# Kernel optimization log

Measured on AMD Instinct MI355X. Metric: run time of the kernel, lower is better.

## Reference

```python
import jax, jax.numpy as jnp
import numpy as np

_K_MASK = float(jnp.finfo(jnp.float32).min)
EPS = 1e-6
B, T, D = 2, 2048, 2048
NH, NKV, HD = 16, 4, 128


def _rope_tables(key):
    # Standard RoPE tables: (B, T, HD) with [freqs, freqs] layout (rotate_half convention)
    inv_freq = 1.0 / (10000.0 ** (np.arange(0, HD, 2, dtype=np.float32) / HD))  # (HD/2,)
    pos = np.arange(T, dtype=np.float32)
    freqs = np.einsum('t,f->tf', pos, inv_freq)              # (T, HD/2)
    emb = np.concatenate([freqs, freqs], axis=-1)            # (T, HD)
    cos = jnp.broadcast_to(jnp.cos(emb)[None], (B, T, HD))
    sin = jnp.broadcast_to(jnp.sin(emb)[None], (B, T, HD))
    return cos, sin


def setup_inputs() -> dict:
    key = jax.random.key(0)
    ks = jax.random.split(key, 6)
    s = 0.02
    cos, sin = _rope_tables(key)
    return {
        'x': jax.random.normal(ks[0], (B, T, D), jnp.float32),
        'cos': cos,
        'sin': sin,
        'wq': jax.random.normal(ks[1], (D, NH * HD * 2), jnp.float32) * s,
        'wk': jax.random.normal(ks[2], (D, NKV * HD), jnp.float32) * s,
        'wv': jax.random.normal(ks[3], (D, NKV * HD), jnp.float32) * s,
        'wo': jax.random.normal(ks[4], (NH * HD, D), jnp.float32) * s,
        'q_norm_w': jnp.ones((HD,), jnp.float32),
        'k_norm_w': jnp.ones((HD,), jnp.float32),
        'segment_ids': jnp.ones((B, T), jnp.int32),
        'position_ids': jnp.broadcast_to(jnp.arange(T, dtype=jnp.int32)[None], (B, T)),
    }


def _rmsnorm(x, w):
    var = jnp.mean(jnp.square(x.astype(jnp.float32)), axis=-1, keepdims=True)
    return (x.astype(jnp.float32) * jax.lax.rsqrt(var + EPS)).astype(x.dtype) * w


def _rotate_half(x):
    x1, x2 = jnp.split(x, 2, axis=-1)
    return jnp.concatenate([-x2, x1], axis=-1)


def _apply_rope(q, k, cos, sin):
    # q: (B, NH, T, HD), k: (B, NKV, T, HD), cos/sin: (B, T, HD)
    c = cos[:, None, :, :]
    s = sin[:, None, :, :]
    q = q * c + _rotate_half(q) * s
    k = k * c + _rotate_half(k) * s
    return q, k


def reference(x, cos, sin, wq, wk, wv, wo, q_norm_w, k_norm_w, segment_ids, position_ids):
    Bx, Tx, _ = x.shape
    n_rep = NH // NKV
    scale = HD ** -0.5

    q_out = (x @ wq).reshape(Bx, Tx, NH, HD * 2)
    query, gate = jnp.split(q_out, 2, axis=-1)         # each (B, T, NH, HD)
    gate = gate.reshape(Bx, Tx, -1)                    # (B, T, NH*HD)
    query = _rmsnorm(query, q_norm_w).transpose(0, 2, 1, 3)   # (B, NH, T, HD)
    key = _rmsnorm((x @ wk).reshape(Bx, Tx, NKV, HD), k_norm_w).transpose(0, 2, 1, 3)
    value = (x @ wv).reshape(Bx, Tx, NKV, HD).transpose(0, 2, 1, 3)

    query, key = _apply_rope(query, key, cos, sin)
    if n_rep > 1:
        key = jnp.repeat(key, n_rep, axis=1)
        value = jnp.repeat(value, n_rep, axis=1)

    attn_logits = jnp.einsum('bhqd,bhkd->bhqk', query, key) * scale
    causal = position_ids[:, :, None] >= position_ids[:, None, :]
    seg = segment_ids[:, :, None] == segment_ids[:, None, :]
    mask = (causal & seg)[:, None, :, :]
    attn_logits = jnp.where(mask, attn_logits, _K_MASK)
    attn_weights = jax.nn.softmax(attn_logits.astype(jnp.float32), axis=-1).astype(attn_logits.dtype)
    attn_out = jnp.einsum('bhqk,bhkd->bhqd', attn_weights, value)
    attn_out = attn_out.transpose(0, 2, 1, 3).reshape(Bx, Tx, -1)  # (B, T, NH*HD)
    attn_out = attn_out * jax.nn.sigmoid(gate)
    return attn_out @ wo
```

## Files before the change

### kernel.cpp

```cpp
#include <hip/hip_runtime.h>

#define AS1 __attribute__((address_space(1)))
#define AS3 __attribute__((address_space(3)))

typedef __bf16 bf16x8 __attribute__((ext_vector_type(8)));
typedef float f32x4 __attribute__((ext_vector_type(4)));
typedef float f32x16 __attribute__((ext_vector_type(16)));
typedef unsigned short us8 __attribute__((ext_vector_type(8)));
typedef unsigned int u32x4 __attribute__((ext_vector_type(4)));

static constexpr int T_ = 2048;
static constexpr int NH_ = 16;
static constexpr int NKV_ = 4;
static constexpr int HD_ = 128;
static constexpr int NQKV_ = 5120;
static constexpr float SL2E_ = 0.12751744f;

static __device__ __forceinline__ unsigned short f2b(float f) {
  unsigned u = __builtin_bit_cast(unsigned, f);
  u += 0x7fffu + ((u >> 16) & 1u);
  return (unsigned short)(u >> 16);
}
static __device__ __forceinline__ void load_lds16(const void* g, void* l) {
  __builtin_amdgcn_global_load_lds((const AS1 unsigned int*)g, (AS3 unsigned int*)l, 16, 0, 0);
}
static __device__ __forceinline__ f32x4 mfma16(bf16x8 a, bf16x8 b, f32x4 c) {
  return __builtin_amdgcn_mfma_f32_16x16x32_bf16(a, b, c, 0, 0, 0);
}
static __device__ __forceinline__ f32x16 mfma32(bf16x8 a, bf16x8 b, f32x16 c) {
  return __builtin_amdgcn_mfma_f32_32x32x16_bf16(a, b, c, 0, 0, 0);
}
static __device__ __forceinline__ unsigned cvtpk(float lo, float hi) {
  unsigned r;
  asm("v_cvt_pk_bf16_f32 %0, %1, %2" : "=v"(r) : "v"(lo), "v"(hi));
  return r;
}
static __device__ __forceinline__ void pl32swap(unsigned& a, unsigned& b) {
  asm("v_permlane32_swap_b32 %0, %1" : "+v"(a), "+v"(b));
}

__global__ __launch_bounds__(256) void conv_bf16_kernel(
    const float* __restrict__ src, unsigned short* __restrict__ dst, int n) {
  int i = (blockIdx.x * 256 + threadIdx.x) * 4;
  if (i >= n) return;
  float4 v = *(const float4*)(src + i);
  ushort4 o;
  o.x = f2b(v.x); o.y = f2b(v.y); o.z = f2b(v.z); o.w = f2b(v.w);
  *(ushort4*)(dst + i) = o;
}

__global__ void tconv_kernel(const float* __restrict__ src, unsigned short* __restrict__ dst,
                             int R, int C, int roff) {
  __shared__ float tile[32][33];
  const int c0 = blockIdx.x * 32, r0 = blockIdx.y * 32;
#pragma unroll
  for (int j = 0; j < 32; j += 8)
    tile[threadIdx.y + j][threadIdx.x] =
        src[(size_t)(r0 + threadIdx.y + j) * C + c0 + threadIdx.x];
  __syncthreads();
#pragma unroll
  for (int j = 0; j < 32; j += 8)
    dst[(size_t)(roff + c0 + threadIdx.y + j) * R + r0 + threadIdx.x] =
        f2b(tile[threadIdx.x][threadIdx.y + j]);
}

__global__ void vtrans_kernel(const float* __restrict__ qkv, unsigned short* __restrict__ Vt) {
  __shared__ unsigned short tile[32][33];
  const int bh = blockIdx.z;
  const int b = bh >> 2, vh = bh & 3;
  const int d0 = blockIdx.x * 32, t0 = blockIdx.y * 32;
#pragma unroll
  for (int j = 0; j < 32; j += 8) {
    const int t = t0 + threadIdx.y + j;
    tile[threadIdx.y + j][threadIdx.x] =
        f2b(qkv[(size_t)(b * T_ + t) * NQKV_ + 4608 + vh * 128 + d0 + threadIdx.x]);
  }
  __syncthreads();
  unsigned short* dst = Vt + (size_t)bh * HD_ * T_;
#pragma unroll
  for (int j = 0; j < 32; j += 8)
    dst[(size_t)(d0 + threadIdx.y + j) * T_ + t0 + threadIdx.x] =
        tile[threadIdx.x][threadIdx.y + j];
}

__global__ __launch_bounds__(256) void gemm_bt_kernel(
    const unsigned short* __restrict__ A, const unsigned short* __restrict__ Bt,
    float* __restrict__ C, int K, int N) {
  __shared__ __align__(16) unsigned short As[128 * 32];
  __shared__ __align__(16) unsigned short Bs[128 * 32];
  const int tid = threadIdx.x;
  const int wid = tid >> 6, lane = tid & 63;
  const int lq = lane & 15, lg = lane >> 4;
  const int wr = wid >> 1, wc = wid & 1;
  const int brow = blockIdx.y * 128, bcol = blockIdx.x * 128;

  f32x4 acc[4][4];
#pragma unroll
  for (int m = 0; m < 4; ++m)
#pragma unroll
    for (int n = 0; n < 4; ++n) acc[m][n] = (f32x4){0.f, 0.f, 0.f, 0.f};

  for (int k0 = 0; k0 < K; k0 += 32) {
#pragma unroll
    for (int i = 0; i < 2; ++i) {
      const int e = (i * 4 + wid) * 512 + lane * 8;
      const int row = e >> 5, col = e & 31;
      load_lds16(A + (size_t)(brow + row) * K + k0 + col, As + (i * 4 + wid) * 512);
      load_lds16(Bt + (size_t)(bcol + row) * K + k0 + col, Bs + (i * 4 + wid) * 512);
    }
    __syncthreads();
    bf16x8 a[4], bb[4];
#pragma unroll
    for (int m = 0; m < 4; ++m)
      a[m] = *(const bf16x8*)&As[(wr * 64 + m * 16 + lq) * 32 + lg * 8];
#pragma unroll
    for (int n = 0; n < 4; ++n)
      bb[n] = *(const bf16x8*)&Bs[(wc * 64 + n * 16 + lq) * 32 + lg * 8];
#pragma unroll
    for (int m = 0; m < 4; ++m)
#pragma unroll
      for (int n = 0; n < 4; ++n) acc[m][n] = mfma16(a[m], bb[n], acc[m][n]);
    __syncthreads();
  }
#pragma unroll
  for (int m = 0; m < 4; ++m)
#pragma unroll
    for (int n = 0; n < 4; ++n)
#pragma unroll
      for (int r = 0; r < 4; ++r)
        C[(size_t)(brow + wr * 64 + m * 16 + lg * 4 + r) * N + bcol + wc * 64 + n * 16 + lq] =
            acc[m][n][r];
}

__global__ __launch_bounds__(256) void postproc_kernel(
    const float* __restrict__ qkv, const float* __restrict__ cosT,
    const float* __restrict__ sinT, const float* __restrict__ qnw,
    const float* __restrict__ knw, unsigned short* __restrict__ Qg,
    unsigned short* __restrict__ Kg) {
  const int row = blockIdx.x;
  const int b = row >> 11, t = row & 2047;
  const float* src = qkv + (size_t)row * NQKV_;
  const int tid = threadIdx.x;
  const int sub = tid & 15;
  const int i0 = sub * 8;
  const bool lo = sub < 8;

  float cs[8], sn[8];
#pragma unroll
  for (int j = 0; j < 8; ++j) {
    cs[j] = cosT[(size_t)row * HD_ + i0 + j];
    sn[j] = sinT[(size_t)row * HD_ + i0 + j];
  }
  {
    const int h = tid >> 4;
    float q[8], ss = 0.f;
#pragma unroll
    for (int j = 0; j < 8; ++j) { q[j] = src[h * 256 + i0 + j]; ss += q[j] * q[j]; }
    ss += __shfl_xor(ss, 1); ss += __shfl_xor(ss, 2);
    ss += __shfl_xor(ss, 4); ss += __shfl_xor(ss, 8);
    const float rms = rsqrtf(ss * (1.f / 128.f) + 1e-6f);
    float qn[8];
#pragma unroll
    for (int j = 0; j < 8; ++j) qn[j] = q[j] * rms * qnw[i0 + j];
    float pr[8];
#pragma unroll
    for (int j = 0; j < 8; ++j) pr[j] = __shfl_xor(qn[j], 8);
    us8 ov;
#pragma unroll
    for (int j = 0; j < 8; ++j) ov[j] = f2b(qn[j] * cs[j] + (lo ? -pr[j] : pr[j]) * sn[j]);
    *(us8*)(Qg + ((size_t)(b * NH_ + h) * T_ + t) * HD_ + i0) = ov;
  }
  if (tid < 64) {
    const int kh = tid >> 4;
    float k[8], ss = 0.f;
#pragma unroll
    for (int j = 0; j < 8; ++j) { k[j] = src[4096 + kh * 128 + i0 + j]; ss += k[j] * k[j]; }
    ss += __shfl_xor(ss, 1); ss += __shfl_xor(ss, 2);
    ss += __shfl_xor(ss, 4); ss += __shfl_xor(ss, 8);
    const float rms = rsqrtf(ss * (1.f / 128.f) + 1e-6f);
    float kn[8];
#pragma unroll
    for (int j = 0; j < 8; ++j) kn[j] = k[j] * rms * knw[i0 + j];
    float pr[8];
#pragma unroll
    for (int j = 0; j < 8; ++j) pr[j] = __shfl_xor(kn[j], 8);
    us8 ov;
#pragma unroll
    for (int j = 0; j < 8; ++j) ov[j] = f2b(kn[j] * cs[j] + (lo ? -pr[j] : pr[j]) * sn[j]);
    *(us8*)(Kg + ((size_t)(b * NKV_ + kh) * T_ + t) * HD_ + i0) = ov;
  }
}

__global__ __launch_bounds__(256, 2) void attn_kernel(
    const unsigned short* __restrict__ Qg, const unsigned short* __restrict__ Kg,
    const unsigned short* __restrict__ Vt, const float* __restrict__ qkv,
    unsigned short* __restrict__ attnb) {
  __shared__ __align__(16) char smem[65536];
  const int i = blockIdx.x;
  const int xi = (i >> 3) & 15;
  const int grp = (i & 7) + ((i >> 7) << 3);
  const int h = grp & 15, b = grp >> 4;
  const int qt = b ? (15 - xi) : xi;
  const int kh = h >> 2;
  const int tid = threadIdx.x, wid = tid >> 6, lane = tid & 63;
  const int lq = lane & 31, hi = lane >> 5;
  const int q0 = qt * 128;
  const int qbase = q0 + wid * 32;
  const int qrow = qbase + lq;

  bf16x8 qf[8];
  const unsigned short* qptr = Qg + ((size_t)(b * NH_ + h) * T_ + qrow) * HD_;
#pragma unroll
  for (int t = 0; t < 8; ++t) qf[t] = *(const bf16x8*)(qptr + t * 16 + hi * 8);

  const char* Kbase = (const char*)(Kg + (size_t)(b * NKV_ + kh) * T_ * HD_);
  const char* Vbase = (const char*)(Vt + (size_t)(b * NKV_ + kh) * HD_ * T_);

  f32x16 o[4];
#pragma unroll
  for (int d = 0; d < 4; ++d)
#pragma unroll
    for (int r = 0; r < 16; ++r) o[d][r] = 0.f;
  float m_r = -1e30f, l_r = 0.f;
  const int nt = 2 * qt + 2;

  auto STAGE = [&](int tt, int c) {
    const int t0 = tt * 64;
    char* kd = smem + c * 32768;
    char* vd = kd + 16384;
#pragma unroll
    for (int j = 0; j < 4; ++j) {
      const int ch = j * 4 + wid;
      const int kv = ch * 4 + (lane >> 4);
      load_lds16(Kbase + (size_t)(t0 + kv) * 256 + (((lane & 15) ^ (kv & 7)) << 4),
                 kd + ch * 1024);
      const int dv = ch * 8 + (lane >> 3);
      load_lds16(Vbase + (size_t)dv * (T_ * 2) + (size_t)t0 * 2 +
                     (((lane & 7) ^ (dv & 7)) << 4),
                 vd + ch * 1024);
    }
  };

  STAGE(0, 0);
  __syncthreads();
  int cur = 0;
  for (int tt = 0; tt < nt; ++tt) {
    const int t0 = tt * 64;
    if (tt + 1 < nt) STAGE(tt + 1, cur ^ 1);
    if (t0 <= qbase + 31) {
      const char* kd = smem + cur * 32768;
      const char* vd = kd + 16384;
      f32x16 sA, sB;
#pragma unroll
      for (int r = 0; r < 16; ++r) { sA[r] = 0.f; sB[r] = 0.f; }
      __builtin_amdgcn_s_setprio(1);
#pragma unroll
      for (int t = 0; t < 8; ++t) {
        const int sw = t * 2 + hi;
        bf16x8 ka = *(const bf16x8*)(kd + lq * 256 + ((sw ^ (lq & 7)) << 4));
        bf16x8 kb = *(const bf16x8*)(kd + (lq + 32) * 256 + ((sw ^ (lq & 7)) << 4));
        sA = mfma32(ka, qf[t], sA);
        sB = mfma32(kb, qf[t], sB);
      }
      __builtin_amdgcn_s_setprio(0);
      float p[32];
      float mx = -1e30f;
      const bool anymask = (t0 + 63 > qbase);
#pragma unroll
      for (int r = 0; r < 16; ++r) {
        const int kv = (r & 3) + ((r >> 2) << 3) + hi * 4;
        float vA = sA[r] * SL2E_;
        float vB = sB[r] * SL2E_;
        if (anymask) {
          if (t0 + kv > qrow) vA = -1e30f;
          if (t0 + kv + 32 > qrow) vB = -1e30f;
        }
        p[r] = vA; p[16 + r] = vB;
        mx = fmaxf(mx, fmaxf(vA, vB));
      }
      mx = fmaxf(mx, __shfl_xor(mx, 32));
      const float mn = fmaxf(m_r, mx);
      const float al = exp2f(m_r - mn);
      float sum = 0.f;
#pragma unroll
      for (int j = 0; j < 32; ++j) { p[j] = exp2f(p[j] - mn); sum += p[j]; }
      sum += __shfl_xor(sum, 32);
      l_r = l_r * al + sum;
      m_r = mn;
#pragma unroll
      for (int d = 0; d < 4; ++d)
#pragma unroll
        for (int r = 0; r < 16; ++r) o[d][r] *= al;
      bf16x8 pf[4];
#pragma unroll
      for (int kt = 0; kt < 4; ++kt) {
        const float* pp = p + kt * 8;
        unsigned a0 = cvtpk(pp[0], pp[1]);
        unsigned a1 = cvtpk(pp[2], pp[3]);
        unsigned b0 = cvtpk(pp[4], pp[5]);
        unsigned b1 = cvtpk(pp[6], pp[7]);
        pl32swap(a0, b0);
        pl32swap(a1, b1);
        u32x4 w = {a0, a1, b0, b1};
        pf[kt] = __builtin_bit_cast(bf16x8, w);
      }
      __builtin_amdgcn_s_setprio(1);
#pragma unroll
      for (int dt = 0; dt < 4; ++dt) {
        const int d = dt * 32 + lq;
#pragma unroll
        for (int kt = 0; kt < 4; ++kt) {
          bf16x8 vf = *(const bf16x8*)(vd + d * 128 + (((kt * 2 + hi) ^ (d & 7)) << 4));
          o[dt] = mfma32(vf, pf[kt], o[dt]);
        }
      }
      __builtin_amdgcn_s_setprio(0);
    }
    __syncthreads();
    cur ^= 1;
  }
  const float inv = 1.f / l_r;
  const float* grow = qkv + (size_t)(b * T_ + qrow) * NQKV_ + h * 256 + 128;
  unsigned short* orow = attnb + (size_t)(b * T_ + qrow) * (NH_ * HD_) + h * HD_;
#pragma unroll
  for (int dt = 0; dt < 4; ++dt)
#pragma unroll
    for (int g = 0; g < 4; ++g) {
      const int d0 = dt * 32 + g * 8 + hi * 4;
      float4 gv = *(const float4*)(grow + d0);
      ushort4 ov;
      ov.x = f2b(o[dt][g * 4 + 0] * inv / (1.f + __expf(-gv.x)));
      ov.y = f2b(o[dt][g * 4 + 1] * inv / (1.f + __expf(-gv.y)));
      ov.z = f2b(o[dt][g * 4 + 2] * inv / (1.f + __expf(-gv.z)));
      ov.w = f2b(o[dt][g * 4 + 3] * inv / (1.f + __expf(-gv.w)));
      *(ushort4*)(orow + d0) = ov;
    }
}

extern "C" void kernel_launch(void* const* d_in, const int* in_sizes, int n_in,
                              void* d_out, int out_size, void* d_ws, size_t ws_size,
                              hipStream_t stream) {
  (void)in_sizes; (void)n_in; (void)out_size; (void)ws_size;
  const float* x    = (const float*)d_in[0];
  const float* cosT = (const float*)d_in[1];
  const float* sinT = (const float*)d_in[2];
  const float* wq   = (const float*)d_in[3];
  const float* wk   = (const float*)d_in[4];
  const float* wv   = (const float*)d_in[5];
  const float* wo   = (const float*)d_in[6];
  const float* qnw  = (const float*)d_in[7];
  const float* knw  = (const float*)d_in[8];
  float* out = (float*)d_out;
  char* ws = (char*)d_ws;

  constexpr size_t OFF_XB    = 0;
  constexpr size_t OFF_WQKVT = OFF_XB    + (size_t)4096 * 2048 * 2;
  constexpr size_t OFF_WOT   = OFF_WQKVT + (size_t)5120 * 2048 * 2;
  constexpr size_t OFF_QKV   = OFF_WOT   + (size_t)2048 * 2048 * 2;
  constexpr size_t OFF_QG    = OFF_QKV   + (size_t)4096 * 5120 * 4;
  constexpr size_t OFF_KG    = OFF_QG    + (size_t)2 * 16 * 2048 * 128 * 2;
  constexpr size_t OFF_VT    = OFF_KG    + (size_t)2 * 4 * 2048 * 128 * 2;
  constexpr size_t OFF_ATTNB = OFF_VT    + (size_t)2 * 4 * 128 * 2048 * 2;

  unsigned short* xb    = (unsigned short*)(ws + OFF_XB);
  unsigned short* wqkvT = (unsigned short*)(ws + OFF_WQKVT);
  unsigned short* woT   = (unsigned short*)(ws + OFF_WOT);
  float*          qkv   = (float*)(ws + OFF_QKV);
  unsigned short* Qg    = (unsigned short*)(ws + OFF_QG);
  unsigned short* Kg    = (unsigned short*)(ws + OFF_KG);
  unsigned short* Vt    = (unsigned short*)(ws + OFF_VT);
  unsigned short* attnb = (unsigned short*)(ws + OFF_ATTNB);

  const int nX = 4096 * 2048;
  conv_bf16_kernel<<<nX / 4 / 256, 256, 0, stream>>>(x, xb, nX);
  tconv_kernel<<<dim3(4096 / 32, 2048 / 32), dim3(32, 8), 0, stream>>>(wq, wqkvT, 2048, 4096, 0);
  tconv_kernel<<<dim3(512 / 32, 2048 / 32), dim3(32, 8), 0, stream>>>(wk, wqkvT, 2048, 512, 4096);
  tconv_kernel<<<dim3(512 / 32, 2048 / 32), dim3(32, 8), 0, stream>>>(wv, wqkvT, 2048, 512, 4608);
  tconv_kernel<<<dim3(2048 / 32, 2048 / 32), dim3(32, 8), 0, stream>>>(wo, woT, 2048, 2048, 0);

  gemm_bt_kernel<<<dim3(5120 / 128, 4096 / 128), 256, 0, stream>>>(xb, wqkvT, qkv, 2048, 5120);

  postproc_kernel<<<4096, 256, 0, stream>>>(qkv, cosT, sinT, qnw, knw, Qg, Kg);
  vtrans_kernel<<<dim3(128 / 32, 2048 / 32, 8), dim3(32, 8), 0, stream>>>(qkv, Vt);

  attn_kernel<<<512, 256, 0, stream>>>(Qg, Kg, Vt, qkv, attnb);

  gemm_bt_kernel<<<dim3(2048 / 128, 4096 / 128), 256, 0, stream>>>(attnb, woT, out, 2048, 2048);
}
```

Baseline: 313.8 us.

## Rewrite GEMM with 128x256 tiles, triple-buffered LDS prefetch and swizzled layout

Replaces the simple single-buffered 128x128 GEMM with an 8-wave 128x256-tile kernel using BK=64. Global-to-LDS loads are prefetched two stages ahead into a triple buffer, with explicit vmcnt waits and raw s_barriers instead of full syncthreads. An XOR swizzle is meant to avoid LDS bank conflicts, and setprio raises MFMA priority. It uses much more LDS, which limits occupancy, and hardcodes K=2048.

```diff
diff --git a/kernel.cpp b/kernel.cpp
--- a/kernel.cpp
+++ b/kernel.cpp
@@ -38,6 +38,7 @@
 static __device__ __forceinline__ void pl32swap(unsigned& a, unsigned& b) {
   asm("v_permlane32_swap_b32 %0, %1" : "+v"(a), "+v"(b));
 }
+#define S_BARRIER() asm volatile("s_barrier" ::: "memory")
 
 __global__ __launch_bounds__(256) void conv_bf16_kernel(
     const float* __restrict__ src, unsigned short* __restrict__ dst, int n) {
@@ -83,16 +84,17 @@
         tile[threadIdx.x][threadIdx.y + j];
 }
 
-__global__ __launch_bounds__(256) void gemm_bt_kernel(
+__global__ __launch_bounds__(512, 2) void gemm_bt8_kernel(
     const unsigned short* __restrict__ A, const unsigned short* __restrict__ Bt,
     float* __restrict__ C, int K, int N) {
-  __shared__ __align__(16) unsigned short As[128 * 32];
-  __shared__ __align__(16) unsigned short Bs[128 * 32];
+  __shared__ __align__(16) unsigned short As[3][128 * 64];
+  __shared__ __align__(16) unsigned short Bs[3][256 * 64];
   const int tid = threadIdx.x;
   const int wid = tid >> 6, lane = tid & 63;
   const int lq = lane & 15, lg = lane >> 4;
-  const int wr = wid >> 1, wc = wid & 1;
-  const int brow = blockIdx.y * 128, bcol = blockIdx.x * 128;
+  const int l8 = lane >> 3, s8 = lane & 7;
+  const int wr = wid >> 2, wc = wid & 3;
+  const int brow = blockIdx.y * 128, bcol = blockIdx.x * 256;
 
   f32x4 acc[4][4];
 #pragma unroll
@@ -100,27 +102,70 @@
 #pragma unroll
     for (int n = 0; n < 4; ++n) acc[m][n] = (f32x4){0.f, 0.f, 0.f, 0.f};
 
-  for (int k0 = 0; k0 < K; k0 += 32) {
-#pragma unroll
-    for (int i = 0; i < 2; ++i) {
-      const int e = (i * 4 + wid) * 512 + lane * 8;
-      const int row = e >> 5, col = e & 31;
-      load_lds16(A + (size_t)(brow + row) * K + k0 + col, As + (i * 4 + wid) * 512);
-      load_lds16(Bt + (size_t)(bcol + row) * K + k0 + col, Bs + (i * 4 + wid) * 512);
-    }
-    __syncthreads();
+  auto STAGE_HALF = [&](int t, int b3t, int half) {
+    const int k0 = t * 64;
+    {
+      const int ca = wid + half * 8;
+      const int row = ca * 8 + l8;
+      load_lds16(A + (size_t)(brow + row) * K + k0 + ((s8 ^ (row & 7)) << 3),
+                 &As[b3t][ca << 9]);
+    }
+#pragma unroll
+    for (int j = 0; j < 2; ++j) {
+      const int cb = wid + half * 16 + (j << 3);
+      const int row = cb * 8 + l8;
+      load_lds16(Bt + (size_t)(bcol + row) * K + k0 + ((s8 ^ (row & 7)) << 3),
+                 &Bs[b3t][cb << 9]);
+    }
+  };
+  auto PHASE_READS = [&](int b3, int ks, bf16x8* a, bf16x8* bb) {
+#pragma unroll
+    for (int m = 0; m < 4; ++m) {
+      const int r = wr * 64 + m * 16 + lq;
+      a[m] = *(const bf16x8*)&As[b3][r * 64 + (((ks * 4 + lg) ^ (r & 7)) << 3)];
+    }
+#pragma unroll
+    for (int n = 0; n < 4; ++n) {
+      const int r = wc * 64 + n * 16 + lq;
+      bb[n] = *(const bf16x8*)&Bs[b3][r * 64 + (((ks * 4 + lg) ^ (r & 7)) << 3)];
+    }
+  };
+  auto DO_MFMA = [&](bf16x8* a, bf16x8* bb) {
+    __builtin_amdgcn_s_setprio(1);
+#pragma unroll
+    for (int m = 0; m < 4; ++m)
+#pragma unroll
+      for (int n = 0; n < 4; ++n) acc[m][n] = mfma16(a[m], bb[n], acc[m][n]);
+    __builtin_amdgcn_s_setprio(0);
+  };
+
+  STAGE_HALF(0, 0, 0); STAGE_HALF(0, 0, 1);
+  STAGE_HALF(1, 1, 0); STAGE_HALF(1, 1, 1);
+  asm volatile("s_waitcnt vmcnt(6)" ::: "memory");
+  S_BARRIER();
+
+  int b3 = 0;
+  for (int t = 0; t < 32; ++t) {
+    const int b3p2 = b3 < 1 ? b3 + 2 : b3 - 1;
     bf16x8 a[4], bb[4];
-#pragma unroll
-    for (int m = 0; m < 4; ++m)
-      a[m] = *(const bf16x8*)&As[(wr * 64 + m * 16 + lq) * 32 + lg * 8];
-#pragma unroll
-    for (int n = 0; n < 4; ++n)
-      bb[n] = *(const bf16x8*)&Bs[(wc * 64 + n * 16 + lq) * 32 + lg * 8];
-#pragma unroll
-    for (int m = 0; m < 4; ++m)
-#pragma unroll
-      for (int n = 0; n < 4; ++n) acc[m][n] = mfma16(a[m], bb[n], acc[m][n]);
-    __syncthreads();
+    PHASE_READS(b3, 0, a, bb);
+    if (t < 30) STAGE_HALF(t + 2, b3p2, 0);
+    S_BARRIER();
+    __builtin_amdgcn_sched_barrier(0);
+    DO_MFMA(a, bb);
+    S_BARRIER();
+    PHASE_READS(b3, 1, a, bb);
+    if (t < 30) STAGE_HALF(t + 2, b3p2, 1);
+    if (t < 30) {
+      asm volatile("s_waitcnt vmcnt(6)" ::: "memory");
+    } else if (t == 30) {
+      asm volatile("s_waitcnt vmcnt(0)" ::: "memory");
+    }
+    S_BARRIER();
+    __builtin_amdgcn_sched_barrier(0);
+    DO_MFMA(a, bb);
+    if (t < 31) S_BARRIER();
+    b3 = b3 < 2 ? b3 + 1 : 0;
   }
 #pragma unroll
   for (int m = 0; m < 4; ++m)
@@ -378,12 +423,12 @@
   tconv_kernel<<<dim3(512 / 32, 2048 / 32), dim3(32, 8), 0, stream>>>(wv, wqkvT, 2048, 512, 4608);
   tconv_kernel<<<dim3(2048 / 32, 2048 / 32), dim3(32, 8), 0, stream>>>(wo, woT, 2048, 2048, 0);
 
-  gemm_bt_kernel<<<dim3(5120 / 128, 4096 / 128), 256, 0, stream>>>(xb, wqkvT, qkv, 2048, 5120);
+  gemm_bt8_kernel<<<dim3(5120 / 256, 4096 / 128), 512, 0, stream>>>(xb, wqkvT, qkv, 2048, 5120);
 
   postproc_kernel<<<4096, 256, 0, stream>>>(qkv, cosT, sinT, qnw, knw, Qg, Kg);
   vtrans_kernel<<<dim3(128 / 32, 2048 / 32, 8), dim3(32, 8), 0, stream>>>(qkv, Vt);
 
   attn_kernel<<<512, 256, 0, stream>>>(Qg, Kg, Vt, qkv, attnb);
 
-  gemm_bt_kernel<<<dim3(2048 / 128, 4096 / 128), 256, 0, stream>>>(attnb, woT, out, 2048, 2048);
-}
+  gemm_bt8_kernel<<<dim3(2048 / 256, 4096 / 128), 512, 0, stream>>>(attnb, woT, out, 2048, 2048);
+}
```

Result: faster. 277.7 us (-11.5%).

## Replace GEMMs with larger-tile, 4-stage pipelined LDS kernels and swizzled grid

Applied to the files above, without the earlier changes.

Both projection GEMMs move from a single-buffered 128x128 tile with 256 threads to 512-thread blocks with larger tiles: 128x320 for the QKV projection and 128x256 for the output projection. Global-to-LDS loads go through a 4-deep ring buffer issued three stages ahead, with explicit vmcnt waits and raw s_barrier in place of __syncthreads. MFMA sections run at raised wave priority, and block IDs are remapped for locality. The aim is to hide memory latency and raise data reuse in the GEMMs, which likely dominate runtime. The cost is more LDS and registers per block and hand-tuned waitcnt logic that is fragile if load counts change.

```diff
diff --git a/kernel.cpp b/kernel.cpp
--- a/kernel.cpp
+++ b/kernel.cpp
@@ -38,6 +38,7 @@
 static __device__ __forceinline__ void pl32swap(unsigned& a, unsigned& b) {
   asm("v_permlane32_swap_b32 %0, %1" : "+v"(a), "+v"(b));
 }
+#define S_BARRIER() asm volatile("s_barrier" ::: "memory")
 
 __global__ __launch_bounds__(256) void conv_bf16_kernel(
     const float* __restrict__ src, unsigned short* __restrict__ dst, int n) {
@@ -83,16 +84,101 @@
         tile[threadIdx.x][threadIdx.y + j];
 }
 
-__global__ __launch_bounds__(256) void gemm_bt_kernel(
+__global__ __launch_bounds__(512, 2) void gemm320_kernel(
     const unsigned short* __restrict__ A, const unsigned short* __restrict__ Bt,
     float* __restrict__ C, int K, int N) {
-  __shared__ __align__(16) unsigned short As[128 * 32];
-  __shared__ __align__(16) unsigned short Bs[128 * 32];
-  const int tid = threadIdx.x;
-  const int wid = tid >> 6, lane = tid & 63;
+  __shared__ __align__(16) unsigned short As[4][128 * 32];
+  __shared__ __align__(16) unsigned short Bs[4][320 * 32];
+  const int nwg = gridDim.x;
+  int bid = blockIdx.x;
+  bid = (bid & 7) * (nwg >> 3) + (bid >> 3);
+  const int gw = N / 320;
+  const int brow = (bid / gw) * 128, bcol = (bid % gw) * 320;
+  const int tid = threadIdx.x, wid = tid >> 6, lane = tid & 63;
   const int lq = lane & 15, lg = lane >> 4;
-  const int wr = wid >> 1, wc = wid & 1;
-  const int brow = blockIdx.y * 128, bcol = blockIdx.x * 128;
+  const int wr = wid >> 2, wc = wid & 3;
+  const int rlane = lane >> 2, plane = lane & 3;
+
+  f32x4 acc[4][5];
+#pragma unroll
+  for (int m = 0; m < 4; ++m)
+#pragma unroll
+    for (int n = 0; n < 5; ++n) acc[m][n] = (f32x4){0.f, 0.f, 0.f, 0.f};
+
+  auto STAGE = [&](int t) {
+    const int k0 = t << 5;
+    const int q = t & 3;
+    load_lds16(A + (size_t)(brow + wid * 16 + rlane) * K + k0 + plane * 8,
+               &As[q][wid << 9]);
+    load_lds16(Bt + (size_t)(bcol + wid * 16 + rlane) * K + k0 + plane * 8,
+               &Bs[q][wid << 9]);
+    load_lds16(Bt + (size_t)(bcol + (wid + 8) * 16 + rlane) * K + k0 + plane * 8,
+               &Bs[q][(wid + 8) << 9]);
+    if (wid < 4)
+      load_lds16(Bt + (size_t)(bcol + (wid + 16) * 16 + rlane) * K + k0 + plane * 8,
+                 &Bs[q][(wid + 16) << 9]);
+  };
+
+  STAGE(0); STAGE(1); STAGE(2);
+  if (wid < 4) asm volatile("s_waitcnt vmcnt(8)" ::: "memory");
+  else         asm volatile("s_waitcnt vmcnt(6)" ::: "memory");
+  S_BARRIER();
+
+  const int NT = K >> 5;
+#pragma unroll 4
+  for (int t = 0; t < NT; ++t) {
+    const int q = t & 3;
+    bf16x8 a[4], b[5];
+#pragma unroll
+    for (int m = 0; m < 4; ++m)
+      a[m] = *(const bf16x8*)&As[q][(wr * 64 + m * 16 + lq) * 32 + lg * 8];
+#pragma unroll
+    for (int n = 0; n < 5; ++n)
+      b[n] = *(const bf16x8*)&Bs[q][(wc * 80 + n * 16 + lq) * 32 + lg * 8];
+    if (t < NT - 3) {
+      STAGE(t + 3);
+      if (wid < 4) asm volatile("s_waitcnt vmcnt(8)" ::: "memory");
+      else         asm volatile("s_waitcnt vmcnt(6)" ::: "memory");
+    } else if (t == NT - 3) {
+      if (wid < 4) asm volatile("s_waitcnt vmcnt(4)" ::: "memory");
+      else         asm volatile("s_waitcnt vmcnt(3)" ::: "memory");
+    } else {
+      asm volatile("s_waitcnt vmcnt(0)" ::: "memory");
+    }
+    S_BARRIER();
+    __builtin_amdgcn_sched_barrier(0);
+    __builtin_amdgcn_s_setprio(1);
+#pragma unroll
+    for (int m = 0; m < 4; ++m)
+#pragma unroll
+      for (int n = 0; n < 5; ++n) acc[m][n] = mfma16(a[m], b[n], acc[m][n]);
+    __builtin_amdgcn_s_setprio(0);
+    S_BARRIER();
+  }
+#pragma unroll
+  for (int m = 0; m < 4; ++m)
+#pragma unroll
+    for (int n = 0; n < 5; ++n)
+#pragma unroll
+      for (int r = 0; r < 4; ++r)
+        C[(size_t)(brow + wr * 64 + m * 16 + lg * 4 + r) * N + bcol + wc * 80 + n * 16 + lq] =
+            acc[m][n][r];
+}
+
+__global__ __launch_bounds__(512, 2) void gemm_bt2_kernel(
+    const unsigned short* __restrict__ A, const unsigned short* __restrict__ Bt,
+    float* __restrict__ C, int K, int N) {
+  __shared__ __align__(16) unsigned short As[4][128 * 32];
+  __shared__ __align__(16) unsigned short Bs[4][256 * 32];
+  const int nwg = gridDim.x;
+  int bid = blockIdx.x;
+  bid = (bid & 7) * (nwg >> 3) + (bid >> 3);
+  const int gw = N >> 8;
+  const int brow = (bid / gw) * 128, bcol = (bid % gw) * 256;
+  const int tid = threadIdx.x, wid = tid >> 6, lane = tid & 63;
+  const int lq = lane & 15, lg = lane >> 4;
+  const int wr = wid >> 2, wc = wid & 3;
+  const int rlane = lane >> 2, plane = lane & 3;
 
   f32x4 acc[4][4];
 #pragma unroll
@@ -100,27 +186,49 @@
 #pragma unroll
     for (int n = 0; n < 4; ++n) acc[m][n] = (f32x4){0.f, 0.f, 0.f, 0.f};
 
-  for (int k0 = 0; k0 < K; k0 += 32) {
-#pragma unroll
-    for (int i = 0; i < 2; ++i) {
-      const int e = (i * 4 + wid) * 512 + lane * 8;
-      const int row = e >> 5, col = e & 31;
-      load_lds16(A + (size_t)(brow + row) * K + k0 + col, As + (i * 4 + wid) * 512);
-      load_lds16(Bt + (size_t)(bcol + row) * K + k0 + col, Bs + (i * 4 + wid) * 512);
+  auto STAGE = [&](int t) {
+    const int k0 = t << 5;
+    const int q = t & 3;
+    load_lds16(A + (size_t)(brow + wid * 16 + rlane) * K + k0 + plane * 8,
+               &As[q][wid << 9]);
+    load_lds16(Bt + (size_t)(bcol + (wid * 2) * 16 + rlane) * K + k0 + plane * 8,
+               &Bs[q][(wid * 2) << 9]);
+    load_lds16(Bt + (size_t)(bcol + (wid * 2 + 1) * 16 + rlane) * K + k0 + plane * 8,
+               &Bs[q][(wid * 2 + 1) << 9]);
+  };
+
+  STAGE(0); STAGE(1); STAGE(2);
+  asm volatile("s_waitcnt vmcnt(6)" ::: "memory");
+  S_BARRIER();
+
+  const int NT = K >> 5;
+#pragma unroll 4
+  for (int t = 0; t < NT; ++t) {
+    const int q = t & 3;
+    bf16x8 a[4], b[4];
+#pragma unroll
+    for (int m = 0; m < 4; ++m)
+      a[m] = *(const bf16x8*)&As[q][(wr * 64 + m * 16 + lq) * 32 + lg * 8];
+#pragma unroll
+    for (int n = 0; n < 4; ++n)
+      b[n] = *(const bf16x8*)&Bs[q][(wc * 64 + n * 16 + lq) * 32 + lg * 8];
+    if (t < NT - 3) {
+      STAGE(t + 3);
+      asm volatile("s_waitcnt vmcnt(6)" ::: "memory");
+    } else if (t == NT - 3) {
+      asm volatile("s_waitcnt vmcnt(3)" ::: "memory");
+    } else {
+      asm volatile("s_waitcnt vmcnt(0)" ::: "memory");
     }
-    __syncthreads();
-    bf16x8 a[4], bb[4];
+    S_BARRIER();
+    __builtin_amdgcn_sched_barrier(0);
+    __builtin_amdgcn_s_setprio(1);
 #pragma unroll
     for (int m = 0; m < 4; ++m)
-      a[m] = *(const bf16x8*)&As[(wr * 64 + m * 16 + lq) * 32 + lg * 8];
-#pragma unroll
-    for (int n = 0; n < 4; ++n)
-      bb[n] = *(const bf16x8*)&Bs[(wc * 64 + n * 16 + lq) * 32 + lg * 8];
-#pragma unroll
-    for (int m = 0; m < 4; ++m)
-#pragma unroll
-      for (int n = 0; n < 4; ++n) acc[m][n] = mfma16(a[m], bb[n], acc[m][n]);
-    __syncthreads();
+#pragma unroll
+      for (int n = 0; n < 4; ++n) acc[m][n] = mfma16(a[m], b[n], acc[m][n]);
+    __builtin_amdgcn_s_setprio(0);
+    S_BARRIER();
   }
 #pragma unroll
   for (int m = 0; m < 4; ++m)
@@ -378,12 +486,12 @@
   tconv_kernel<<<dim3(512 / 32, 2048 / 32), dim3(32, 8), 0, stream>>>(wv, wqkvT, 2048, 512, 4608);
   tconv_kernel<<<dim3(2048 / 32, 2048 / 32), dim3(32, 8), 0, stream>>>(wo, woT, 2048, 2048, 0);
 
-  gemm_bt_kernel<<<dim3(5120 / 128, 4096 / 128), 256, 0, stream>>>(xb, wqkvT, qkv, 2048, 5120);
+  gemm320_kernel<<<512, 512, 0, stream>>>(xb, wqkvT, qkv, 2048, 5120);
 
   postproc_kernel<<<4096, 256, 0, stream>>>(qkv, cosT, sinT, qnw, knw, Qg, Kg);
   vtrans_kernel<<<dim3(128 / 32, 2048 / 32, 8), dim3(32, 8), 0, stream>>>(qkv, Vt);
 
   attn_kernel<<<512, 256, 0, stream>>>(Qg, Kg, Vt, qkv, attnb);
 
-  gemm_bt_kernel<<<dim3(2048 / 128, 4096 / 128), 256, 0, stream>>>(attnb, woT, out, 2048, 2048);
-}
+  gemm_bt2_kernel<<<256, 512, 0, stream>>>(attnb, woT, out, 2048, 2048);
+}
```

Result: faster. 285.5 us (-9.0%).

## Store QKV projection as bf16 and remap GEMM tiles for XCD locality

Applied to the files above, without the earlier changes.

The QKV GEMM now writes bf16 instead of fp32, which halves the intermediate buffer. The postproc, V-transpose and attention gate reads consume bf16 directly with vector loads. Both GEMMs use a 1D grid with a block-id swizzle that groups tiles across the 8 XCDs, and the LDS staging load uses a new row/column mapping. Rounding the pre-norm Q/K, V and gate values to bf16 adds precision loss.

```diff
diff --git a/kernel.cpp b/kernel.cpp
--- a/kernel.cpp
+++ b/kernel.cpp
@@ -20,6 +20,10 @@
   unsigned u = __builtin_bit_cast(unsigned, f);
   u += 0x7fffu + ((u >> 16) & 1u);
   return (unsigned short)(u >> 16);
+}
+static __device__ __forceinline__ float b2f(unsigned short h) {
+  unsigned u = ((unsigned)h) << 16;
+  return __builtin_bit_cast(float, u);
 }
 static __device__ __forceinline__ void load_lds16(const void* g, void* l) {
   __builtin_amdgcn_global_load_lds((const AS1 unsigned int*)g, (AS3 unsigned int*)l, 16, 0, 0);
@@ -64,7 +68,8 @@
         f2b(tile[threadIdx.x][threadIdx.y + j]);
 }
 
-__global__ void vtrans_kernel(const float* __restrict__ qkv, unsigned short* __restrict__ Vt) {
+__global__ void vtrans_kernel(const unsigned short* __restrict__ qkv,
+                              unsigned short* __restrict__ Vt) {
   __shared__ unsigned short tile[32][33];
   const int bh = blockIdx.z;
   const int b = bh >> 2, vh = bh & 3;
@@ -73,7 +78,7 @@
   for (int j = 0; j < 32; j += 8) {
     const int t = t0 + threadIdx.y + j;
     tile[threadIdx.y + j][threadIdx.x] =
-        f2b(qkv[(size_t)(b * T_ + t) * NQKV_ + 4608 + vh * 128 + d0 + threadIdx.x]);
+        qkv[(size_t)(b * T_ + t) * NQKV_ + 4608 + vh * 128 + d0 + threadIdx.x];
   }
   __syncthreads();
   unsigned short* dst = Vt + (size_t)bh * HD_ * T_;
@@ -83,16 +88,21 @@
         tile[threadIdx.x][threadIdx.y + j];
 }
 
-__global__ __launch_bounds__(256) void gemm_bt_kernel(
+template <int BF16OUT>
+__global__ __launch_bounds__(256) void gemm97_kernel(
     const unsigned short* __restrict__ A, const unsigned short* __restrict__ Bt,
-    float* __restrict__ C, int K, int N) {
+    void* __restrict__ Cv, int K, int N) {
   __shared__ __align__(16) unsigned short As[128 * 32];
   __shared__ __align__(16) unsigned short Bs[128 * 32];
-  const int tid = threadIdx.x;
-  const int wid = tid >> 6, lane = tid & 63;
+  const int nwg = gridDim.x;
+  int bid = blockIdx.x;
+  bid = (bid & 7) * (nwg >> 3) + (bid >> 3);
+  const int gw = N >> 7;
+  const int brow = (bid / gw) * 128, bcol = (bid % gw) * 128;
+  const int tid = threadIdx.x, wid = tid >> 6, lane = tid & 63;
   const int lq = lane & 15, lg = lane >> 4;
   const int wr = wid >> 1, wc = wid & 1;
-  const int brow = blockIdx.y * 128, bcol = blockIdx.x * 128;
+  const int srow = lane >> 2, spc = lane & 3;
 
   f32x4 acc[4][4];
 #pragma unroll
@@ -102,24 +112,23 @@
 
   for (int k0 = 0; k0 < K; k0 += 32) {
 #pragma unroll
-    for (int i = 0; i < 2; ++i) {
-      const int e = (i * 4 + wid) * 512 + lane * 8;
-      const int row = e >> 5, col = e & 31;
-      load_lds16(A + (size_t)(brow + row) * K + k0 + col, As + (i * 4 + wid) * 512);
-      load_lds16(Bt + (size_t)(bcol + row) * K + k0 + col, Bs + (i * 4 + wid) * 512);
+    for (int j = 0; j < 2; ++j) {
+      const int ch = wid + j * 4;
+      load_lds16(A + (size_t)(brow + ch * 16 + srow) * K + k0 + spc * 8, As + (ch << 9));
+      load_lds16(Bt + (size_t)(bcol + ch * 16 + srow) * K + k0 + spc * 8, Bs + (ch << 9));
     }
     __syncthreads();
-    bf16x8 a[4], bb[4];
+    bf16x8 a[4], b[4];
 #pragma unroll
     for (int m = 0; m < 4; ++m)
       a[m] = *(const bf16x8*)&As[(wr * 64 + m * 16 + lq) * 32 + lg * 8];
 #pragma unroll
     for (int n = 0; n < 4; ++n)
-      bb[n] = *(const bf16x8*)&Bs[(wc * 64 + n * 16 + lq) * 32 + lg * 8];
+      b[n] = *(const bf16x8*)&Bs[(wc * 64 + n * 16 + lq) * 32 + lg * 8];
 #pragma unroll
     for (int m = 0; m < 4; ++m)
 #pragma unroll
-      for (int n = 0; n < 4; ++n) acc[m][n] = mfma16(a[m], bb[n], acc[m][n]);
+      for (int n = 0; n < 4; ++n) acc[m][n] = mfma16(a[m], b[n], acc[m][n]);
     __syncthreads();
   }
 #pragma unroll
@@ -127,19 +136,25 @@
 #pragma unroll
     for (int n = 0; n < 4; ++n)
 #pragma unroll
-      for (int r = 0; r < 4; ++r)
-        C[(size_t)(brow + wr * 64 + m * 16 + lg * 4 + r) * N + bcol + wc * 64 + n * 16 + lq] =
-            acc[m][n][r];
+      for (int r = 0; r < 4; ++r) {
+        const size_t idx =
+            (size_t)(brow + wr * 64 + m * 16 + lg * 4 + r) * N + bcol + wc * 64 + n * 16 + lq;
+        if constexpr (BF16OUT) {
+          ((unsigned short*)Cv)[idx] = f2b(acc[m][n][r]);
+        } else {
+          ((float*)Cv)[idx] = acc[m][n][r];
+        }
+      }
 }
 
 __global__ __launch_bounds__(256) void postproc_kernel(
-    const float* __restrict__ qkv, const float* __restrict__ cosT,
+    const unsigned short* __restrict__ qkv, const float* __restrict__ cosT,
     const float* __restrict__ sinT, const float* __restrict__ qnw,
     const float* __restrict__ knw, unsigned short* __restrict__ Qg,
     unsigned short* __restrict__ Kg) {
   const int row = blockIdx.x;
   const int b = row >> 11, t = row & 2047;
-  const float* src = qkv + (size_t)row * NQKV_;
+  const unsigned short* src = qkv + (size_t)row * NQKV_;
   const int tid = threadIdx.x;
   const int sub = tid & 15;
   const int i0 = sub * 8;
@@ -153,9 +168,10 @@
   }
   {
     const int h = tid >> 4;
+    us8 qv = *(const us8*)(src + h * 256 + i0);
     float q[8], ss = 0.f;
 #pragma unroll
-    for (int j = 0; j < 8; ++j) { q[j] = src[h * 256 + i0 + j]; ss += q[j] * q[j]; }
+    for (int j = 0; j < 8; ++j) { q[j] = b2f(qv[j]); ss += q[j] * q[j]; }
     ss += __shfl_xor(ss, 1); ss += __shfl_xor(ss, 2);
     ss += __shfl_xor(ss, 4); ss += __shfl_xor(ss, 8);
     const float rms = rsqrtf(ss * (1.f / 128.f) + 1e-6f);
@@ -172,9 +188,10 @@
   }
   if (tid < 64) {
     const int kh = tid >> 4;
+    us8 kv8 = *(const us8*)(src + 4096 + kh * 128 + i0);
     float k[8], ss = 0.f;
 #pragma unroll
-    for (int j = 0; j < 8; ++j) { k[j] = src[4096 + kh * 128 + i0 + j]; ss += k[j] * k[j]; }
+    for (int j = 0; j < 8; ++j) { k[j] = b2f(kv8[j]); ss += k[j] * k[j]; }
     ss += __shfl_xor(ss, 1); ss += __shfl_xor(ss, 2);
     ss += __shfl_xor(ss, 4); ss += __shfl_xor(ss, 8);
     const float rms = rsqrtf(ss * (1.f / 128.f) + 1e-6f);
@@ -193,7 +210,7 @@
 
 __global__ __launch_bounds__(256, 2) void attn_kernel(
     const unsigned short* __restrict__ Qg, const unsigned short* __restrict__ Kg,
-    const unsigned short* __restrict__ Vt, const float* __restrict__ qkv,
+    const unsigned short* __restrict__ Vt, const unsigned short* __restrict__ qkv,
     unsigned short* __restrict__ attnb) {
   __shared__ __align__(16) char smem[65536];
   const int i = blockIdx.x;
@@ -320,19 +337,19 @@
     cur ^= 1;
   }
   const float inv = 1.f / l_r;
-  const float* grow = qkv + (size_t)(b * T_ + qrow) * NQKV_ + h * 256 + 128;
+  const unsigned short* grow = qkv + (size_t)(b * T_ + qrow) * NQKV_ + h * 256 + 128;
   unsigned short* orow = attnb + (size_t)(b * T_ + qrow) * (NH_ * HD_) + h * HD_;
 #pragma unroll
   for (int dt = 0; dt < 4; ++dt)
 #pragma unroll
     for (int g = 0; g < 4; ++g) {
       const int d0 = dt * 32 + g * 8 + hi * 4;
-      float4 gv = *(const float4*)(grow + d0);
+      ushort4 gv = *(const ushort4*)(grow + d0);
       ushort4 ov;
-      ov.x = f2b(o[dt][g * 4 + 0] * inv / (1.f + __expf(-gv.x)));
-      ov.y = f2b(o[dt][g * 4 + 1] * inv / (1.f + __expf(-gv.y)));
-      ov.z = f2b(o[dt][g * 4 + 2] * inv / (1.f + __expf(-gv.z)));
-      ov.w = f2b(o[dt][g * 4 + 3] * inv / (1.f + __expf(-gv.w)));
+      ov.x = f2b(o[dt][g * 4 + 0] * inv / (1.f + __expf(-b2f(gv.x))));
+      ov.y = f2b(o[dt][g * 4 + 1] * inv / (1.f + __expf(-b2f(gv.y))));
+      ov.z = f2b(o[dt][g * 4 + 2] * inv / (1.f + __expf(-b2f(gv.z))));
+      ov.w = f2b(o[dt][g * 4 + 3] * inv / (1.f + __expf(-b2f(gv.w))));
       *(ushort4*)(orow + d0) = ov;
     }
 }
@@ -357,7 +374,7 @@
   constexpr size_t OFF_WQKVT = OFF_XB    + (size_t)4096 * 2048 * 2;
   constexpr size_t OFF_WOT   = OFF_WQKVT + (size_t)5120 * 2048 * 2;
   constexpr size_t OFF_QKV   = OFF_WOT   + (size_t)2048 * 2048 * 2;
-  constexpr size_t OFF_QG    = OFF_QKV   + (size_t)4096 * 5120 * 4;
+  constexpr size_t OFF_QG    = OFF_QKV   + (size_t)4096 * 5120 * 2;
   constexpr size_t OFF_KG    = OFF_QG    + (size_t)2 * 16 * 2048 * 128 * 2;
   constexpr size_t OFF_VT    = OFF_KG    + (size_t)2 * 4 * 2048 * 128 * 2;
   constexpr size_t OFF_ATTNB = OFF_VT    + (size_t)2 * 4 * 128 * 2048 * 2;
@@ -365,7 +382,7 @@
   unsigned short* xb    = (unsigned short*)(ws + OFF_XB);
   unsigned short* wqkvT = (unsigned short*)(ws + OFF_WQKVT);
   unsigned short* woT   = (unsigned short*)(ws + OFF_WOT);
-  float*          qkv   = (float*)(ws + OFF_QKV);
+  unsigned short* qkv   = (unsigned short*)(ws + OFF_QKV);
   unsigned short* Qg    = (unsigned short*)(ws + OFF_QG);
   unsigned short* Kg    = (unsigned short*)(ws + OFF_KG);
   unsigned short* Vt    = (unsigned short*)(ws + OFF_VT);
@@ -378,12 +395,12 @@
   tconv_kernel<<<dim3(512 / 32, 2048 / 32), dim3(32, 8), 0, stream>>>(wv, wqkvT, 2048, 512, 4608);
   tconv_kernel<<<dim3(2048 / 32, 2048 / 32), dim3(32, 8), 0, stream>>>(wo, woT, 2048, 2048, 0);
 
-  gemm_bt_kernel<<<dim3(5120 / 128, 4096 / 128), 256, 0, stream>>>(xb, wqkvT, qkv, 2048, 5120);
+  gemm97_kernel<1><<<1280, 256, 0, stream>>>(xb, wqkvT, (void*)qkv, 2048, 5120);
 
   postproc_kernel<<<4096, 256, 0, stream>>>(qkv, cosT, sinT, qnw, knw, Qg, Kg);
   vtrans_kernel<<<dim3(128 / 32, 2048 / 32, 8), dim3(32, 8), 0, stream>>>(qkv, Vt);
 
   attn_kernel<<<512, 256, 0, stream>>>(Qg, Kg, Vt, qkv, attnb);
 
-  gemm_bt_kernel<<<dim3(2048 / 128, 4096 / 128), 256, 0, stream>>>(attnb, woT, out, 2048, 2048);
-}
+  gemm97_kernel<0><<<512, 256, 0, stream>>>(attnb, woT, (void*)out, 2048, 2048);
+}
```

Result: faster. 306.0 us (-2.5%).
